# Kernel tuning notes

Measured on AMD Instinct MI355X. Metric: run time of the kernel, lower is better.

## Reference

```python
import jax, jax.numpy as jnp
import numpy as np

N = 4096
IN_F = 256
OUT_F = 64
H = 4
NEG_SLOPE = 0.2


def setup_inputs() -> dict:
    key = jax.random.key(0)
    k1, k2, k3, k4 = jax.random.split(key, 4)
    x = jax.random.normal(k1, (N, IN_F), dtype=jnp.float32)
    adj = jax.random.randint(k2, (N, N), 0, 2).astype(jnp.float32)
    # Xavier-uniform init, matching nn.init.xavier_uniform_
    limW = float(np.sqrt(6.0 / (IN_F + OUT_F)))
    W = jax.random.uniform(k3, (H, IN_F, OUT_F), minval=-limW, maxval=limW, dtype=jnp.float32)
    lima = float(np.sqrt(6.0 / (2 * OUT_F + 1)))
    a = jax.random.uniform(k4, (H, 2 * OUT_F, 1), minval=-lima, maxval=lima, dtype=jnp.float32)
    return {"x": x, "adj": adj, "W": W, "a": a}


def reference(x, adj, W, a):
    # x: [N, in], adj: [N, N], W: [H, in, out], a: [H, 2*out, 1]
    n = x.shape[0]
    h, _, fo = W.shape
    Wh = jnp.einsum('nd,hdo->nho', x, W)  # [N, H, O]
    # Additive score: a^T [Wh_i || Wh_j] = (a_src . Wh_i) + (a_dst . Wh_j)
    a_src = a[:, :fo, 0]   # [H, O]
    a_dst = a[:, fo:, 0]   # [H, O]
    s_i = jnp.einsum('nho,ho->nh', Wh, a_src)  # [N, H]
    s_j = jnp.einsum('nho,ho->nh', Wh, a_dst)  # [N, H]
    e = jax.nn.leaky_relu(s_i[:, None, :] + s_j[None, :, :], NEG_SLOPE)  # [N, N, H]
    # Add self-loops on the diagonal, mask non-edges
    idx = jnp.arange(n)
    adj_sl = adj.at[idx, idx].set(1.0)
    mask = (adj_sl != 0)[:, :, None]  # [N, N, 1]
    e_masked = jnp.where(mask, e, -jnp.inf)
    attention = jax.nn.softmax(e_masked, axis=1)  # softmax over neighbors j
    # (dropout is identity in eval mode)
    h_prime = jnp.einsum('ijh,jho->iho', attention, Wh)  # [N, H, O]
    return h_prime.reshape(n, h * fo)  # concat=True
```

## Files before the change

kernel.cpp:

```cpp
#include <hip/hip_runtime.h>
#include <hip/hip_bf16.h>

typedef float    f32x4 __attribute__((ext_vector_type(4)));
typedef _Float16 f16x8 __attribute__((ext_vector_type(8)));
typedef _Float16 f16x4 __attribute__((ext_vector_type(4)));
typedef __fp16   fp16x2 __attribute__((ext_vector_type(2)));

#define NN 4096
#define INF_ 256
#define OUTF 64
#define NH 4
#define NSPL 8
#define NGRP 128
#define LOG2E 1.4426950408889634f

__device__ __forceinline__ unsigned enc_f32(float f) {
    unsigned u = __float_as_uint(f);
    return (u & 0x80000000u) ? ~u : (u | 0x80000000u);
}
__device__ __forceinline__ float dec_f32(unsigned u) {
    return (u & 0x80000000u) ? __uint_as_float(u ^ 0x80000000u)
                             : __uint_as_float(~u);
}

__global__ __launch_bounds__(256) void kW_tr(const float* __restrict__ W,
                                             _Float16* __restrict__ wBh,
                                             _Float16* __restrict__ wBl,
                                             unsigned* __restrict__ smax)
{
    const int b = blockIdx.x;
    const int h = b >> 3, ks = b & 7;
    const int t = threadIdx.x;
    const int ob = t >> 6, lane = t & 63;
    const int row16 = lane & 15, quad = lane >> 4;

    const float* wp = W + (size_t)h*INF_*OUTF + (ks*32 + quad*8)*OUTF + ob*16 + row16;
    f16x8 vh, vl;
#pragma unroll
    for (int e = 0; e < 8; ++e) {
        float v = wp[e*OUTF];
        _Float16 hi = (_Float16)v;
        vh[e] = hi;
        vl[e] = (_Float16)(v - (float)hi);
    }
    const int idx = ((h*8 + ks)*4 + ob)*64 + lane;
    reinterpret_cast<f16x8*>(wBh)[idx] = vh;
    reinterpret_cast<f16x8*>(wBl)[idx] = vl;

    if (b == 0 && t < NH) smax[t] = 0u;
}

__global__ __launch_bounds__(256) void k01(
    const float* __restrict__ adj, unsigned* __restrict__ pack,
    const float* __restrict__ x, const _Float16* __restrict__ wBh,
    const _Float16* __restrict__ wBl, const float* __restrict__ a,
    _Float16* __restrict__ whB, float* __restrict__ s_src,
    float* __restrict__ s_dst, unsigned* __restrict__ smax)
{
    __shared__ float red[4][4][64][4];
    __shared__ float red2_s[4][16];
    __shared__ float red2_d[4][16];

    if (blockIdx.x >= 1024) {
        const int r    = blockIdx.x - 1024;
        const int w    = threadIdx.x >> 6;
        const int lane = threadIdx.x & 63;
        const float* rowp = adj + (size_t)r * NN + w * 1024;

        f32x4 v[4];
#pragma unroll
        for (int i = 0; i < 4; ++i)
            v[i] = *reinterpret_cast<const f32x4*>(rowp + i*256 + lane*4);

#pragma unroll
        for (int i = 0; i < 4; ++i) {
            unsigned nib = (unsigned)(v[i][0] != 0.f)
                         | ((unsigned)(v[i][1] != 0.f) << 1)
                         | ((unsigned)(v[i][2] != 0.f) << 2)
                         | ((unsigned)(v[i][3] != 0.f) << 3);
            unsigned val = nib << ((lane & 7) * 4);
            val |= __shfl_xor(val, 1);
            val |= __shfl_xor(val, 2);
            val |= __shfl_xor(val, 4);
            if ((lane & 7) == 0) {
                const int wi = w*32 + i*8 + (lane >> 3);
                if (wi == (r >> 5)) val |= 1u << (r & 31);
                pack[r*128 + wi] = val;
            }
        }
        return;
    }

    const int b = blockIdx.x;
    const int h = b >> 8, rg = b & 255;
    const int n0 = rg * 16;
    const int w = threadIdx.x >> 6, lane = threadIdx.x & 63;
    const int row16 = lane & 15, quad = lane >> 4;

    f32x4 accA[4], accB[4], accC[4];
#pragma unroll
    for (int ob = 0; ob < 4; ++ob) {
        accA[ob] = (f32x4){0,0,0,0};
        accB[ob] = (f32x4){0,0,0,0};
        accC[ob] = (f32x4){0,0,0,0};
    }

    const float* xp = x + (size_t)(n0 + row16)*INF_ + quad*8;
    const f16x8* WH = reinterpret_cast<const f16x8*>(wBh) + (h*8*4)*64 + lane;
    const f16x8* WL = reinterpret_cast<const f16x8*>(wBl) + (h*8*4)*64 + lane;

#pragma unroll
    for (int ksl = 0; ksl < 2; ++ksl) {
        const int ks = w*2 + ksl;
        float4 xv0 = *reinterpret_cast<const float4*>(xp + ks*32);
        float4 xv1 = *reinterpret_cast<const float4*>(xp + ks*32 + 4);
        const float xv[8] = {xv0.x,xv0.y,xv0.z,xv0.w,xv1.x,xv1.y,xv1.z,xv1.w};
        f16x8 Ah, Al;
#pragma unroll
        for (int e = 0; e < 8; ++e) {
            _Float16 hi = (_Float16)xv[e];
            Ah[e] = hi;
            Al[e] = (_Float16)(xv[e] - (float)hi);
        }
#pragma unroll
        for (int ob = 0; ob < 4; ++ob) {
            f16x8 bh = WH[(ks*4 + ob)*64];
            f16x8 bl = WL[(ks*4 + ob)*64];
            accA[ob] = __builtin_amdgcn_mfma_f32_16x16x32_f16(Ah, bh, accA[ob], 0, 0, 0);
            accB[ob] = __builtin_amdgcn_mfma_f32_16x16x32_f16(Al, bh, accB[ob], 0, 0, 0);
            accC[ob] = __builtin_amdgcn_mfma_f32_16x16x32_f16(Ah, bl, accC[ob], 0, 0, 0);
        }
    }

#pragma unroll
    for (int ob = 0; ob < 4; ++ob) {
        f32x4 p = accA[ob] + accB[ob] + accC[ob];
        *reinterpret_cast<f32x4*>(&red[w][ob][lane][0]) = p;
    }
    __syncthreads();

    const int myob = w;
    f32x4 acc = *reinterpret_cast<const f32x4*>(&red[0][myob][lane][0]);
#pragma unroll
    for (int ws2 = 1; ws2 < 4; ++ws2)
        acc += *reinterpret_cast<const f32x4*>(&red[ws2][myob][lane][0]);

    {
        const int jblk = n0 >> 5;
        const int qb   = ((n0 & 16) >> 3) + (quad >> 1);
        const int e0   = (quad & 1) * 4;
        f16x4 st;
#pragma unroll
        for (int q = 0; q < 4; ++q) st[q] = (_Float16)acc[q];
        const size_t off = (((size_t)(h*NGRP + jblk)*4 + myob)*64 + qb*16 + row16)*8 + e0;
        *reinterpret_cast<f16x4*>(whB + off) = st;
    }

    const float as = a[h*128 + myob*16 + row16];
    const float ad = a[h*128 + 64 + myob*16 + row16];
#pragma unroll
    for (int q = 0; q < 4; ++q) {
        float vs = acc[q] * as;
        float vd = acc[q] * ad;
#pragma unroll
        for (int m = 1; m <= 8; m <<= 1) {
            vs += __shfl_xor(vs, m);
            vd += __shfl_xor(vd, m);
        }
        if (row16 == 0) {
            red2_s[myob][quad*4 + q] = vs;
            red2_d[myob][quad*4 + q] = vd;
        }
    }
    __syncthreads();

    if (threadIdx.x < 16) {
        const int r = threadIdx.x;
        const float vs = red2_s[0][r] + red2_s[1][r] + red2_s[2][r] + red2_s[3][r];
        const float vd = red2_d[0][r] + red2_d[1][r] + red2_d[2][r] + red2_d[3][r];
        const float sd = LOG2E * vd;
        s_src[h*NN + n0 + r] = LOG2E * vs;
        s_dst[h*NN + n0 + r] = sd;
        float vmax = sd;
#pragma unroll
        for (int m = 1; m <= 8; m <<= 1) vmax = fmaxf(vmax, __shfl_xor(vmax, m));
        if (r == 0) atomicMax(&smax[h], enc_f32(vmax));
    }
}

template <int USE_PART>
__global__ __launch_bounds__(256, 4) void k3_attn(
    const unsigned* __restrict__ pack, const _Float16* __restrict__ whB,
    const float* __restrict__ s_src, const float* __restrict__ s_dst,
    const unsigned* __restrict__ smax_enc,
    float* __restrict__ outp, float* __restrict__ l_ws)
{
    constexpr int STEPS_ = NN / NSPL / 32;

    const int b      = blockIdx.x;
    const int jsplit = b % NSPL;
    const int r2     = b / NSPL;
    const int hh     = r2 & 3;
    const int grp    = r2 >> 2;
    const int w      = threadIdx.x >> 6;
    const int lane   = threadIdx.x & 63;
    const int row16  = lane & 15;
    const int quad   = lane >> 4;
    const int i0     = (grp * 4 + w) * 32;
    const int jb0    = jsplit * (NN / NSPL);
    const int jblk0  = jb0 >> 5;

    const float sm = dec_f32(smax_enc[hh]);
    float A1[2], A2[2];
    const unsigned* prow[2];
#pragma unroll
    for (int f = 0; f < 2; ++f) {
        const int ir = i0 + f*16 + row16;
        const float s_i = s_src[hh*NN + ir];
        const float zb  = s_i + sm;
        const float mb  = fmaxf(zb, 0.2f * zb);
        A1[f] = s_i - mb;
        A2[f] = 0.2f * s_i - mb;
        prow[f] = pack + ir*128 + jblk0;
    }

    f32x4 acc[2][4];
    f32x4 accl[2];
#pragma unroll
    for (int f = 0; f < 2; ++f) {
        accl[f] = (f32x4){0,0,0,0};
#pragma unroll
        for (int ob = 0; ob < 4; ++ob) acc[f][ob] = (f32x4){0,0,0,0};
    }

    f16x8 ones;
#pragma unroll
    for (int e = 0; e < 8; ++e) ones[e] = (_Float16)1.0f;

    const _Float16* bB  = whB + (size_t)(hh*NGRP + jblk0)*2048 + lane*8;
    const float*    sdp = s_dst + hh*NN + jb0 + quad*8;

    f16x8 B0 = *reinterpret_cast<const f16x8*>(bB);
    f16x8 B1 = *reinterpret_cast<const f16x8*>(bB + 512);
    f16x8 B2 = *reinterpret_cast<const f16x8*>(bB + 1024);
    f16x8 B3 = *reinterpret_cast<const f16x8*>(bB + 1536);
    unsigned msk0 = prow[0][0], msk1 = prow[1][0];
    float4 sj0 = *reinterpret_cast<const float4*>(sdp);
    float4 sj1 = *reinterpret_cast<const float4*>(sdp + 4);

    for (int s = 0; s < STEPS_; ++s) {
        const _Float16* bn = bB + (s+1)*2048;
        f16x8 nB0 = *reinterpret_cast<const f16x8*>(bn);
        f16x8 nB1 = *reinterpret_cast<const f16x8*>(bn + 512);
        f16x8 nB2 = *reinterpret_cast<const f16x8*>(bn + 1024);
        f16x8 nB3 = *reinterpret_cast<const f16x8*>(bn + 1536);
        unsigned nmsk0 = prow[0][s+1], nmsk1 = prow[1][s+1];
        float4 nsj0 = *reinterpret_cast<const float4*>(sdp + (s+1)*32);
        float4 nsj1 = *reinterpret_cast<const float4*>(sdp + (s+1)*32 + 4);

        const float sjv[8] = {sj0.x,sj0.y,sj0.z,sj0.w,sj1.x,sj1.y,sj1.z,sj1.w};
        float us[8];
#pragma unroll
        for (int e = 0; e < 8; ++e) us[e] = 0.2f * sjv[e];

        const unsigned mskf[2] = {msk0, msk1};
#pragma unroll
        for (int f = 0; f < 2; ++f) {
            const unsigned mm8 = (mskf[f] >> (quad * 8)) & 0xffu;
            float pe[8];
#pragma unroll
            for (int e = 0; e < 8; ++e) {
                float t1 = A1[f] + sjv[e];
                float t2 = A2[f] + us[e];
                float p  = __builtin_amdgcn_exp2f(fmaxf(t1, t2));
                pe[e] = (mm8 & (1u << e)) ? p : 0.0f;
            }
            union { f16x8 v8; fp16x2 p2[4]; } pa;
#pragma unroll
            for (int e2 = 0; e2 < 4; ++e2)
                pa.p2[e2] = __builtin_amdgcn_cvt_pkrtz(pe[2*e2], pe[2*e2+1]);

            acc[f][0] = __builtin_amdgcn_mfma_f32_16x16x32_f16(pa.v8, B0, acc[f][0], 0, 0, 0);
            acc[f][1] = __builtin_amdgcn_mfma_f32_16x16x32_f16(pa.v8, B1, acc[f][1], 0, 0, 0);
            acc[f][2] = __builtin_amdgcn_mfma_f32_16x16x32_f16(pa.v8, B2, acc[f][2], 0, 0, 0);
            acc[f][3] = __builtin_amdgcn_mfma_f32_16x16x32_f16(pa.v8, B3, acc[f][3], 0, 0, 0);
            accl[f]   = __builtin_amdgcn_mfma_f32_16x16x32_f16(pa.v8, ones, accl[f], 0, 0, 0);
        }

        B0 = nB0; B1 = nB1; B2 = nB2; B3 = nB3;
        msk0 = nmsk0; msk1 = nmsk1;
        sj0 = nsj0; sj1 = nsj1;
    }

#pragma unroll
    for (int f = 0; f < 2; ++f) {
        if (row16 == 0) {
#pragma unroll
            for (int q = 0; q < 4; ++q) {
                const int ir = i0 + f*16 + quad*4 + q;
                if (USE_PART) l_ws[(jsplit*NH + hh)*NN + ir] = accl[f][q];
                else          atomicAdd(&l_ws[hh*NN + ir], accl[f][q]);
            }
        }
    }
    if (USE_PART) {
        float* pw = outp + ((size_t)((jsplit*NH + hh)*NGRP + (i0 >> 5))) * 2048 + lane;
#pragma unroll
        for (int f = 0; f < 2; ++f)
#pragma unroll
            for (int ob = 0; ob < 4; ++ob)
#pragma unroll
                for (int q = 0; q < 4; ++q)
                    pw[((f*4 + ob)*4 + q)*64] = acc[f][ob][q];
    } else {
#pragma unroll
        for (int f = 0; f < 2; ++f)
#pragma unroll
            for (int ob = 0; ob < 4; ++ob)
#pragma unroll
                for (int q = 0; q < 4; ++q) {
                    const int grow = i0 + f*16 + quad*4 + q;
                    const int gcol = hh*OUTF + ob*16 + row16;
                    atomicAdd(&outp[(size_t)grow*256 + gcol], acc[f][ob][q]);
                }
    }
}

__global__ __launch_bounds__(256) void k4_part(const float* __restrict__ part,
                                               const float* __restrict__ l_ws,
                                               float* __restrict__ out)
{
    const int idx = blockIdx.x * 256 + threadIdx.x;
    const int n = idx >> 6, c4 = idx & 63;
    const int h = c4 >> 4, k = c4 & 15;
    const int g = n >> 5, f = (n >> 4) & 1, quad = (n >> 2) & 3, q = n & 3;
    const int ob = k >> 2, lb = quad*16 + (k & 3)*4;

    float L = 0.f;
    f32x4 v = {0,0,0,0};
#pragma unroll
    for (int sp = 0; sp < NSPL; ++sp) {
        L += l_ws[(sp*NH + h)*NN + n];
        const float* p = part + ((size_t)((sp*NH + h)*NGRP + g))*2048
                              + ((f*4 + ob)*4 + q)*64 + lb;
        v += *reinterpret_cast<const f32x4*>(p);
    }
    const float inv = 1.0f / L;
    *reinterpret_cast<f32x4*>(out + (size_t)n*256 + c4*4) = v * inv;
}

__global__ __launch_bounds__(256) void k4_atomic(float* __restrict__ out,
                                                 const float* __restrict__ l_acc)
{
    const int idx = blockIdx.x * 256 + threadIdx.x;
    const int n = idx >> 6, c4 = idx & 63, h = c4 >> 4;
    const float inv = 1.0f / l_acc[h*NN + n];
    f32x4 v = *reinterpret_cast<f32x4*>(out + (size_t)n*256 + c4*4);
    *reinterpret_cast<f32x4*>(out + (size_t)n*256 + c4*4) = v * inv;
}

extern "C" void kernel_launch(void* const* d_in, const int* in_sizes, int n_in,
                              void* d_out, int out_size, void* d_ws, size_t ws_size,
                              hipStream_t stream)
{
    const float* x   = (const float*)d_in[0];
    const float* adj = (const float*)d_in[1];
    const float* W   = (const float*)d_in[2];
    const float* a   = (const float*)d_in[3];
    float* out = (float*)d_out;

    char* ws = (char*)d_ws;
    _Float16* whB  = (_Float16*)ws;
    unsigned* pack = (unsigned*)(ws + (2u<<20));
    _Float16* wBh  = (_Float16*)(ws + (4u<<20));
    _Float16* wBl  = (_Float16*)(ws + (4u<<20) + (128u<<10));
    float* s_src   = (float*)(ws + (4u<<20) + (256u<<10));
    float* s_dst   = (float*)(ws + (4u<<20) + (320u<<10));
    unsigned* smax = (unsigned*)(ws + (4u<<20) + (384u<<10));
    float* l_ws    = (float*)(ws + (4u<<20) + (385u<<10));
    float* part    = (float*)(ws + (4u<<20) + (897u<<10));

    const size_t need = (4u<<20) + (897u<<10) + (size_t)NSPL * NN * 256 * 4;

    kW_tr<<<32, 256, 0, stream>>>(W, wBh, wBl, smax);
    k01  <<<1024 + NN, 256, 0, stream>>>(adj, pack, x, wBh, wBl, a,
                                         whB, s_src, s_dst, smax);

    if (ws_size >= need) {
        k3_attn<1><<<1024, 256, 0, stream>>>(pack, whB, s_src, s_dst, smax, part, l_ws);
        k4_part<<<1024, 256, 0, stream>>>(part, l_ws, out);
    } else {
        (void)hipMemsetAsync(d_out, 0, (size_t)out_size * sizeof(float), stream);
        (void)hipMemsetAsync(l_ws, 0, NH * NN * sizeof(float), stream);
        k3_attn<0><<<1024, 256, 0, stream>>>(pack, whB, s_src, s_dst, smax, out, l_ws);
        k4_atomic<<<1024, 256, 0, stream>>>(out, l_ws);
    }
}
```

Baseline: 78.81 us.

## Read fp32 adjacency directly in attention kernel instead of prepacked bitmask

Drops the adjacency bit-packing pass from the first projection kernel and has the attention kernel load raw fp32 adjacency rows, testing for non-zero entries and the diagonal self-loop inline. This removes a separate pass and the packed-mask workspace. In exchange, each head's attention blocks re-read the 64MB fp32 adjacency, relying on cache reuse across heads, and per-thread load volume in the inner loop grows. The occupancy hint on the attention kernel is also removed.

```diff
diff --git a/kernel.cpp b/kernel.cpp
--- a/kernel.cpp
+++ b/kernel.cpp
@@ -50,8 +50,7 @@
     if (b == 0 && t < NH) smax[t] = 0u;
 }
 
-__global__ __launch_bounds__(256) void k01(
-    const float* __restrict__ adj, unsigned* __restrict__ pack,
+__global__ __launch_bounds__(256) void k1m(
     const float* __restrict__ x, const _Float16* __restrict__ wBh,
     const _Float16* __restrict__ wBl, const float* __restrict__ a,
     _Float16* __restrict__ whB, float* __restrict__ s_src,
@@ -60,36 +59,6 @@
     __shared__ float red[4][4][64][4];
     __shared__ float red2_s[4][16];
     __shared__ float red2_d[4][16];
-
-    if (blockIdx.x >= 1024) {
-        const int r    = blockIdx.x - 1024;
-        const int w    = threadIdx.x >> 6;
-        const int lane = threadIdx.x & 63;
-        const float* rowp = adj + (size_t)r * NN + w * 1024;
-
-        f32x4 v[4];
-#pragma unroll
-        for (int i = 0; i < 4; ++i)
-            v[i] = *reinterpret_cast<const f32x4*>(rowp + i*256 + lane*4);
-
-#pragma unroll
-        for (int i = 0; i < 4; ++i) {
-            unsigned nib = (unsigned)(v[i][0] != 0.f)
-                         | ((unsigned)(v[i][1] != 0.f) << 1)
-                         | ((unsigned)(v[i][2] != 0.f) << 2)
-                         | ((unsigned)(v[i][3] != 0.f) << 3);
-            unsigned val = nib << ((lane & 7) * 4);
-            val |= __shfl_xor(val, 1);
-            val |= __shfl_xor(val, 2);
-            val |= __shfl_xor(val, 4);
-            if ((lane & 7) == 0) {
-                const int wi = w*32 + i*8 + (lane >> 3);
-                if (wi == (r >> 5)) val |= 1u << (r & 31);
-                pack[r*128 + wi] = val;
-            }
-        }
-        return;
-    }
 
     const int b = blockIdx.x;
     const int h = b >> 8, rg = b & 255;
@@ -189,8 +158,8 @@
 }
 
 template <int USE_PART>
-__global__ __launch_bounds__(256, 4) void k3_attn(
-    const unsigned* __restrict__ pack, const _Float16* __restrict__ whB,
+__global__ __launch_bounds__(256) void k3_attn(
+    const float* __restrict__ adj, const _Float16* __restrict__ whB,
     const float* __restrict__ s_src, const float* __restrict__ s_dst,
     const unsigned* __restrict__ smax_enc,
     float* __restrict__ outp, float* __restrict__ l_ws)
@@ -211,17 +180,19 @@
     const int jblk0  = jb0 >> 5;
 
     const float sm = dec_f32(smax_enc[hh]);
-    float A1[2], A2[2];
-    const unsigned* prow[2];
+    float A1c[2], A2c[2];
+    const float* ap[2];
+    int dloc[2];
 #pragma unroll
     for (int f = 0; f < 2; ++f) {
         const int ir = i0 + f*16 + row16;
         const float s_i = s_src[hh*NN + ir];
         const float zb  = s_i + sm;
         const float mb  = fmaxf(zb, 0.2f * zb);
-        A1[f] = s_i - mb;
-        A2[f] = 0.2f * s_i - mb;
-        prow[f] = pack + ir*128 + jblk0;
+        A1c[f] = s_i - mb;
+        A2c[f] = 0.2f * s_i - mb;
+        ap[f]   = adj + (size_t)ir*NN + jb0 + quad*8;
+        dloc[f] = ir - (jb0 + quad*8);
     }
 
     f32x4 acc[2][4];
@@ -244,36 +215,46 @@
     f16x8 B1 = *reinterpret_cast<const f16x8*>(bB + 512);
     f16x8 B2 = *reinterpret_cast<const f16x8*>(bB + 1024);
     f16x8 B3 = *reinterpret_cast<const f16x8*>(bB + 1536);
-    unsigned msk0 = prow[0][0], msk1 = prow[1][0];
+    f32x4 Aj[2][2], nAj[2][2];
+#pragma unroll
+    for (int f = 0; f < 2; ++f) {
+        Aj[f][0] = *reinterpret_cast<const f32x4*>(ap[f]);
+        Aj[f][1] = *reinterpret_cast<const f32x4*>(ap[f] + 4);
+    }
     float4 sj0 = *reinterpret_cast<const float4*>(sdp);
     float4 sj1 = *reinterpret_cast<const float4*>(sdp + 4);
 
     for (int s = 0; s < STEPS_; ++s) {
-        const _Float16* bn = bB + (s+1)*2048;
+        const int sn = (s + 1) & (STEPS_ - 1);
+        const _Float16* bn = bB + sn*2048;
         f16x8 nB0 = *reinterpret_cast<const f16x8*>(bn);
         f16x8 nB1 = *reinterpret_cast<const f16x8*>(bn + 512);
         f16x8 nB2 = *reinterpret_cast<const f16x8*>(bn + 1024);
         f16x8 nB3 = *reinterpret_cast<const f16x8*>(bn + 1536);
-        unsigned nmsk0 = prow[0][s+1], nmsk1 = prow[1][s+1];
-        float4 nsj0 = *reinterpret_cast<const float4*>(sdp + (s+1)*32);
-        float4 nsj1 = *reinterpret_cast<const float4*>(sdp + (s+1)*32 + 4);
+#pragma unroll
+        for (int f = 0; f < 2; ++f) {
+            nAj[f][0] = *reinterpret_cast<const f32x4*>(ap[f] + sn*32);
+            nAj[f][1] = *reinterpret_cast<const f32x4*>(ap[f] + sn*32 + 4);
+        }
+        float4 nsj0 = *reinterpret_cast<const float4*>(sdp + sn*32);
+        float4 nsj1 = *reinterpret_cast<const float4*>(sdp + sn*32 + 4);
 
         const float sjv[8] = {sj0.x,sj0.y,sj0.z,sj0.w,sj1.x,sj1.y,sj1.z,sj1.w};
         float us[8];
 #pragma unroll
         for (int e = 0; e < 8; ++e) us[e] = 0.2f * sjv[e];
 
-        const unsigned mskf[2] = {msk0, msk1};
 #pragma unroll
         for (int f = 0; f < 2; ++f) {
-            const unsigned mm8 = (mskf[f] >> (quad * 8)) & 0xffu;
+            const int dls = dloc[f] - s*32;
             float pe[8];
 #pragma unroll
             for (int e = 0; e < 8; ++e) {
-                float t1 = A1[f] + sjv[e];
-                float t2 = A2[f] + us[e];
+                const float av = (e < 4) ? Aj[f][0][e] : Aj[f][1][e-4];
+                float t1 = A1c[f] + sjv[e];
+                float t2 = A2c[f] + us[e];
                 float p  = __builtin_amdgcn_exp2f(fmaxf(t1, t2));
-                pe[e] = (mm8 & (1u << e)) ? p : 0.0f;
+                pe[e] = ((av != 0.0f) || (dls == e)) ? p : 0.0f;
             }
             union { f16x8 v8; fp16x2 p2[4]; } pa;
 #pragma unroll
@@ -288,7 +269,11 @@
         }
 
         B0 = nB0; B1 = nB1; B2 = nB2; B3 = nB3;
-        msk0 = nmsk0; msk1 = nmsk1;
+#pragma unroll
+        for (int f = 0; f < 2; ++f) {
+            Aj[f][0] = nAj[f][0];
+            Aj[f][1] = nAj[f][1];
+        }
         sj0 = nsj0; sj1 = nsj1;
     }
 
@@ -371,7 +356,6 @@
 
     char* ws = (char*)d_ws;
     _Float16* whB  = (_Float16*)ws;
-    unsigned* pack = (unsigned*)(ws + (2u<<20));
     _Float16* wBh  = (_Float16*)(ws + (4u<<20));
     _Float16* wBl  = (_Float16*)(ws + (4u<<20) + (128u<<10));
     float* s_src   = (float*)(ws + (4u<<20) + (256u<<10));
@@ -383,16 +367,15 @@
     const size_t need = (4u<<20) + (897u<<10) + (size_t)NSPL * NN * 256 * 4;
 
     kW_tr<<<32, 256, 0, stream>>>(W, wBh, wBl, smax);
-    k01  <<<1024 + NN, 256, 0, stream>>>(adj, pack, x, wBh, wBl, a,
-                                         whB, s_src, s_dst, smax);
+    k1m  <<<1024, 256, 0, stream>>>(x, wBh, wBl, a, whB, s_src, s_dst, smax);
 
     if (ws_size >= need) {
-        k3_attn<1><<<1024, 256, 0, stream>>>(pack, whB, s_src, s_dst, smax, part, l_ws);
+        k3_attn<1><<<1024, 256, 0, stream>>>(adj, whB, s_src, s_dst, smax, part, l_ws);
         k4_part<<<1024, 256, 0, stream>>>(part, l_ws, out);
     } else {
         (void)hipMemsetAsync(d_out, 0, (size_t)out_size * sizeof(float), stream);
         (void)hipMemsetAsync(l_ws, 0, NH * NN * sizeof(float), stream);
-        k3_attn<0><<<1024, 256, 0, stream>>>(pack, whB, s_src, s_dst, smax, out, l_ws);
+        k3_attn<0><<<1024, 256, 0, stream>>>(adj, whB, s_src, s_dst, smax, out, l_ws);
         k4_atomic<<<1024, 256, 0, stream>>>(out, l_ws);
     }
 }
```

Result: slower. 93.41 us (+18.5%).
